# Performance work log

Measured on AMD Instinct MI355X. Metric: run time of the kernel, lower is better.

## Reference

```python
import jax, jax.numpy as jnp
import numpy as np

NEG_SLOPE = 0.2  # PyG GATConv default LeakyReLU negative slope
NUM_GRAPHS = 256


def gat_conv(x, edge_src, edge_dst, W, att_src, att_dst, bias):
    """PyG-style GATConv. x:[N,Fin], W:[H*C,Fin], att_*:[H,C], bias:[H*C]."""
    N = x.shape[0]
    H, C = att_src.shape
    h = (x @ W.T).reshape(N, H, C)                       # [N,H,C]
    a_src = jnp.sum(h * att_src, axis=-1)                # [N,H]
    a_dst = jnp.sum(h * att_dst, axis=-1)                # [N,H]
    e = jax.nn.leaky_relu(a_src[edge_src] + a_dst[edge_dst], NEG_SLOPE)  # [E,H]
    # segment softmax over edges sharing the same destination node
    m = jax.ops.segment_max(e, edge_dst, num_segments=N)
    ex = jnp.exp(e - m[edge_dst])
    den = jax.ops.segment_sum(ex, edge_dst, num_segments=N)
    alpha = ex / (den[edge_dst] + 1e-16)                 # [E,H]
    out = jax.ops.segment_sum(h[edge_src] * alpha[..., None], edge_dst,
                              num_segments=N)            # [N,H,C]
    return out.reshape(N, H * C) + bias


def setup_inputs() -> dict:
    key = jax.random.key(0)
    ks = jax.random.split(key, 16)
    N, E, Fin = 20000, 320000, 128
    H1, C1 = 8, 64          # conv1: heads=8, hidden_dim1=64 -> concat 512
    D1 = H1 * C1            # 512
    D2 = 128                # hidden_dim2, conv2 heads=1
    OUT = 2
    s = lambda k, shp, fan: jax.random.normal(k, shp, jnp.float32) * (1.0 / np.sqrt(fan))
    x = jax.random.normal(ks[0], (N, Fin), jnp.float32)
    edge_index = jax.random.randint(ks[1], (2, E), 0, N, jnp.int32)
    batch = jnp.sort(jax.random.randint(ks[2], (N,), 0, NUM_GRAPHS, jnp.int32))
    return {
        "x": x, "edge_index": edge_index, "batch": batch,
        "W1": s(ks[3], (D1, Fin), Fin), "att_src1": s(ks[4], (H1, C1), C1),
        "att_dst1": s(ks[5], (H1, C1), C1), "b1": jnp.zeros((D1,), jnp.float32),
        "W2": s(ks[6], (D2, D1), D1), "att_src2": s(ks[7], (1, D2), D2),
        "att_dst2": s(ks[8], (1, D2), D2), "b2": jnp.zeros((D2,), jnp.float32),
        "w_attn": s(ks[9], (D2, 1), D2), "b_attn": jnp.zeros((1,), jnp.float32),
        "w_mask": s(ks[10], (D2, 1), D2), "b_mask": jnp.zeros((1,), jnp.float32),
        "W_out": s(ks[11], (OUT, D2), D2), "b_out": jnp.zeros((OUT,), jnp.float32),
    }


def reference(x, edge_index, batch, W1, att_src1, att_dst1, b1,
              W2, att_src2, att_dst2, b2, w_attn, b_attn, w_mask, b_mask,
              W_out, b_out):
    N = x.shape[0]
    loops = jnp.arange(N, dtype=edge_index.dtype)
    src = jnp.concatenate([edge_index[0], loops])  # PyG add_self_loops=True
    dst = jnp.concatenate([edge_index[1], loops])

    h = gat_conv(x, src, dst, W1, att_src1, att_dst1, b1)   # [N, 512]
    h = jax.nn.relu(h)                                      # dropout = identity (eval)
    h = gat_conv(h, src, dst, W2, att_src2, att_dst2, b2)   # [N, 128]
    h = jax.nn.relu(h)

    # attention pooling over graphs in the batch
    attn_scores = h @ w_attn + b_attn                       # [N,1]
    node_mask = jax.nn.sigmoid(h @ w_mask + b_mask)         # [N,1]
    weighted = h * (attn_scores * node_mask)                # [N,128]
    pooled = jax.ops.segment_sum(weighted, batch, num_segments=NUM_GRAPHS)
    return pooled @ W_out.T + b_out                         # [256, 2]
```

## Files before the change

### kernel.cpp

```cpp
#include <hip/hip_runtime.h>
#include <math.h>


#define NEG_SLOPE 0.2f

using bf16x8 = __attribute__((ext_vector_type(8))) __bf16;
using f32x4  = __attribute__((ext_vector_type(4))) float;

__device__ __forceinline__ ushort f2bf(float f) {
    unsigned u = __float_as_uint(f);
    unsigned r = (u + 0x7FFFu + ((u >> 16) & 1u)) >> 16;
    return (ushort)r;
}
__device__ __forceinline__ unsigned pack2(float a, float b) {
    return (unsigned)f2bf(a) | ((unsigned)f2bf(b) << 16);
}
__device__ __forceinline__ void unpack8(uint4 u, float* f) {
    f[0] = __uint_as_float(u.x << 16); f[1] = __uint_as_float(u.x & 0xFFFF0000u);
    f[2] = __uint_as_float(u.y << 16); f[3] = __uint_as_float(u.y & 0xFFFF0000u);
    f[4] = __uint_as_float(u.z << 16); f[5] = __uint_as_float(u.z & 0xFFFF0000u);
    f[6] = __uint_as_float(u.w << 16); f[7] = __uint_as_float(u.w & 0xFFFF0000u);
}
__device__ __forceinline__ void unpack4(uint2 u, float* f) {
    f[0] = __uint_as_float(u.x << 16); f[1] = __uint_as_float(u.x & 0xFFFF0000u);
    f[2] = __uint_as_float(u.y << 16); f[3] = __uint_as_float(u.y & 0xFFFF0000u);
}

__global__ __launch_bounds__(256) void cvt_bf16(const float* __restrict__ in,
                                                ushort* __restrict__ out, int n4) {
    int i = blockIdx.x * 256 + threadIdx.x;
    if (i >= n4) return;
    float4 v = ((const float4*)in)[i];
    uint2 o;
    o.x = pack2(v.x, v.y);
    o.y = pack2(v.z, v.w);
    ((uint2*)out)[i] = o;
}

#define LDSB 40
__global__ __launch_bounds__(256) void gemm_mfma(const ushort* __restrict__ A,
                                                 const ushort* __restrict__ B,
                                                 ushort* __restrict__ C,
                                                 int M, int N, int K) {
    __shared__ ushort As[128 * LDSB];
    __shared__ ushort Bs[128 * LDSB];
    int t = threadIdx.x;
    int wave = t >> 6, lane = t & 63;
    int quad = lane >> 4, l16 = lane & 15;
    int m0 = blockIdx.x * 128;
    int n0 = blockIdx.y * 128;
    int wm = (wave & 1) * 64;
    int wn = (wave >> 1) * 64;
    int srow = t >> 1;
    int sseg = (t & 1) * 16;
    f32x4 acc[4][4] = {};
    for (int k0 = 0; k0 < K; k0 += 32) {
        uint4 av0, av1, bv0, bv1;
        {
            int grow = m0 + srow;
            if (grow < M) {
                const uint4* gp = (const uint4*)(A + (size_t)grow * K + k0 + sseg);
                av0 = gp[0]; av1 = gp[1];
            } else {
                av0 = make_uint4(0, 0, 0, 0); av1 = av0;
            }
            const uint4* gq = (const uint4*)(B + (size_t)(n0 + srow) * K + k0 + sseg);
            bv0 = gq[0]; bv1 = gq[1];
        }
        __syncthreads();
        *(uint4*)&As[srow * LDSB + sseg]     = av0;
        *(uint4*)&As[srow * LDSB + sseg + 8] = av1;
        *(uint4*)&Bs[srow * LDSB + sseg]     = bv0;
        *(uint4*)&Bs[srow * LDSB + sseg + 8] = bv1;
        __syncthreads();
        bf16x8 af[4], bf[4];
#pragma unroll
        for (int i = 0; i < 4; ++i)
            af[i] = *(const bf16x8*)&As[(wm + i * 16 + l16) * LDSB + quad * 8];
#pragma unroll
        for (int j = 0; j < 4; ++j)
            bf[j] = *(const bf16x8*)&Bs[(wn + j * 16 + l16) * LDSB + quad * 8];
#pragma unroll
        for (int i = 0; i < 4; ++i)
#pragma unroll
            for (int j = 0; j < 4; ++j)
                acc[i][j] = __builtin_amdgcn_mfma_f32_16x16x32_bf16(
                    af[i], bf[j], acc[i][j], 0, 0, 0);
    }
#pragma unroll
    for (int i = 0; i < 4; ++i) {
#pragma unroll
        for (int r = 0; r < 4; ++r) {
            int grow = m0 + wm + i * 16 + quad * 4 + r;
            if (grow < M) {
#pragma unroll
                for (int j = 0; j < 4; ++j) {
                    int gcol = n0 + wn + j * 16 + l16;
                    C[(size_t)grow * N + gcol] = f2bf(acc[i][j][r]);
                }
            }
        }
    }
}

__global__ __launch_bounds__(256) void scores1(const ushort* __restrict__ h1,
                                               const float* __restrict__ att_s,
                                               const float* __restrict__ att_d,
                                               float* __restrict__ a1s,
                                               float* __restrict__ a1d, int N) {
    int node = blockIdx.x * 4 + (threadIdx.x >> 6);
    if (node >= N) return;
    int lane = threadIdx.x & 63;
    uint4 u = *(const uint4*)(h1 + (size_t)node * 512 + lane * 8);
    float h[8];
    unpack8(u, h);
    const float4* sp = (const float4*)(att_s + lane * 8);
    const float4* dp = (const float4*)(att_d + lane * 8);
    float4 s0 = sp[0], s1 = sp[1], d0 = dp[0], d1 = dp[1];
    float ps = h[0] * s0.x + h[1] * s0.y + h[2] * s0.z + h[3] * s0.w +
               h[4] * s1.x + h[5] * s1.y + h[6] * s1.z + h[7] * s1.w;
    float pd = h[0] * d0.x + h[1] * d0.y + h[2] * d0.z + h[3] * d0.w +
               h[4] * d1.x + h[5] * d1.y + h[6] * d1.z + h[7] * d1.w;
#pragma unroll
    for (int off = 1; off < 8; off <<= 1) {
        ps += __shfl_xor(ps, off);
        pd += __shfl_xor(pd, off);
    }
    if ((lane & 7) == 0) {
        a1s[node * 8 + (lane >> 3)] = ps;
        a1d[node * 8 + (lane >> 3)] = pd;
    }
}

__global__ void count_edges(const int* __restrict__ dst, int* cnt, int E) {
    int e = blockIdx.x * 256 + threadIdx.x;
    if (e < E) atomicAdd(&cnt[dst[e]], 1);
}

__global__ __launch_bounds__(1024) void scan_offsets(const int* cnt, int* row_start,
                                                     int* cursor, int N) {
    __shared__ int sm[1024];
    int t = threadIdx.x;
    int per = (N + 1023) / 1024;
    int beg = t * per;
    int end = beg + per; if (end > N) end = N;
    int sum = 0;
    for (int i = beg; i < end; ++i) sum += cnt[i];
    sm[t] = sum;
    __syncthreads();
    for (int off = 1; off < 1024; off <<= 1) {
        int add = (t >= off) ? sm[t - off] : 0;
        __syncthreads();
        sm[t] += add;
        __syncthreads();
    }
    int run = sm[t] - sum;
    for (int i = beg; i < end; ++i) {
        int c = cnt[i];
        row_start[i] = run;
        cursor[i] = run;
        run += c;
    }
    if (t == 1023) row_start[N] = run;
}

__global__ void fill_edges(const int* __restrict__ src, const int* __restrict__ dst,
                           int* cursor, int* __restrict__ srcs, int E) {
    int e = blockIdx.x * 256 + threadIdx.x;
    if (e < E) {
        int pos = atomicAdd(&cursor[dst[e]], 1);
        srcs[pos] = src[e];
    }
}

__global__ __launch_bounds__(256) void agg1(const ushort* __restrict__ h1,
                                            const float* __restrict__ a1s,
                                            const float* __restrict__ a1d,
                                            const int* __restrict__ row_start,
                                            const int* __restrict__ srcs,
                                            const float* __restrict__ b1,
                                            ushort* __restrict__ r1, int N) {
    int node = blockIdx.x * 4 + (threadIdx.x >> 6);
    if (node >= N) return;
    int lane = threadIdx.x & 63;
    int head = lane >> 3;
    int f0 = lane * 8;
    int pbeg = row_start[node], pend = row_start[node + 1];
    float ad = a1d[node * 8 + head];
    float es = a1s[node * 8 + head] + ad;
    es = es > 0.f ? es : NEG_SLOPE * es;
    float ex_self = __expf(es);
    float den = ex_self;
    float q[8];
    unpack8(*(const uint4*)(h1 + (size_t)node * 512 + f0), q);
    float acc[8];
#pragma unroll
    for (int j = 0; j < 8; ++j) acc[j] = ex_self * q[j];
    int p = pbeg;
    for (; p + 4 <= pend; p += 4) {
        int s0 = srcs[p + 0];
        int s1 = srcs[p + 1];
        int s2 = srcs[p + 2];
        int s3 = srcs[p + 3];
        uint4 u0 = *(const uint4*)(h1 + (size_t)s0 * 512 + f0);
        uint4 u1 = *(const uint4*)(h1 + (size_t)s1 * 512 + f0);
        uint4 u2 = *(const uint4*)(h1 + (size_t)s2 * 512 + f0);
        uint4 u3 = *(const uint4*)(h1 + (size_t)s3 * 512 + f0);
        float as0 = a1s[s0 * 8 + head];
        float as1 = a1s[s1 * 8 + head];
        float as2 = a1s[s2 * 8 + head];
        float as3 = a1s[s3 * 8 + head];
        float e0 = as0 + ad; e0 = e0 > 0.f ? e0 : NEG_SLOPE * e0;
        float e1 = as1 + ad; e1 = e1 > 0.f ? e1 : NEG_SLOPE * e1;
        float e2 = as2 + ad; e2 = e2 > 0.f ? e2 : NEG_SLOPE * e2;
        float e3 = as3 + ad; e3 = e3 > 0.f ? e3 : NEG_SLOPE * e3;
        float x0 = __expf(e0), x1 = __expf(e1), x2 = __expf(e2), x3 = __expf(e3);
        den += (x0 + x1) + (x2 + x3);
        float v[8];
        unpack8(u0, v);
#pragma unroll
        for (int j = 0; j < 8; ++j) acc[j] += x0 * v[j];
        unpack8(u1, v);
#pragma unroll
        for (int j = 0; j < 8; ++j) acc[j] += x1 * v[j];
        unpack8(u2, v);
#pragma unroll
        for (int j = 0; j < 8; ++j) acc[j] += x2 * v[j];
        unpack8(u3, v);
#pragma unroll
        for (int j = 0; j < 8; ++j) acc[j] += x3 * v[j];
    }
    for (; p < pend; ++p) {
        int s = srcs[p];
        float e = a1s[s * 8 + head] + ad;
        e = e > 0.f ? e : NEG_SLOPE * e;
        float ex = __expf(e);
        den += ex;
        float v[8];
        unpack8(*(const uint4*)(h1 + (size_t)s * 512 + f0), v);
#pragma unroll
        for (int j = 0; j < 8; ++j) acc[j] += ex * v[j];
    }
    float rden = 1.0f / (den + 1e-16f);
    const float4* bp = (const float4*)(b1 + f0);
    float4 b0 = bp[0], b1v = bp[1];
    float o[8];
    o[0] = fmaxf(acc[0] * rden + b0.x, 0.f);
    o[1] = fmaxf(acc[1] * rden + b0.y, 0.f);
    o[2] = fmaxf(acc[2] * rden + b0.z, 0.f);
    o[3] = fmaxf(acc[3] * rden + b0.w, 0.f);
    o[4] = fmaxf(acc[4] * rden + b1v.x, 0.f);
    o[5] = fmaxf(acc[5] * rden + b1v.y, 0.f);
    o[6] = fmaxf(acc[6] * rden + b1v.z, 0.f);
    o[7] = fmaxf(acc[7] * rden + b1v.w, 0.f);
    uint4 ov;
    ov.x = pack2(o[0], o[1]); ov.y = pack2(o[2], o[3]);
    ov.z = pack2(o[4], o[5]); ov.w = pack2(o[6], o[7]);
    *(uint4*)(r1 + (size_t)node * 512 + f0) = ov;
}

__global__ __launch_bounds__(256) void scores2(const ushort* __restrict__ h2,
                                               const float* __restrict__ att_s,
                                               const float* __restrict__ att_d,
                                               float* __restrict__ a2s,
                                               float* __restrict__ a2d, int N) {
    int node = blockIdx.x * 4 + (threadIdx.x >> 6);
    if (node >= N) return;
    int lane = threadIdx.x & 63;
    unsigned u = *(const unsigned*)(h2 + (size_t)node * 128 + lane * 2);
    float h0 = __uint_as_float(u << 16), h1v = __uint_as_float(u & 0xFFFF0000u);
    float2 s = *(const float2*)(att_s + lane * 2);
    float2 d = *(const float2*)(att_d + lane * 2);
    float ps = h0 * s.x + h1v * s.y;
    float pd = h0 * d.x + h1v * d.y;
#pragma unroll
    for (int off = 1; off < 64; off <<= 1) {
        ps += __shfl_xor(ps, off);
        pd += __shfl_xor(pd, off);
    }
    if (lane == 0) { a2s[node] = ps; a2d[node] = pd; }
}

__global__ __launch_bounds__(256) void agg2(const ushort* __restrict__ h2,
                                            const float* __restrict__ a2s,
                                            const float* __restrict__ a2d,
                                            const int* __restrict__ row_start,
                                            const int* __restrict__ srcs,
                                            const float* __restrict__ b2,
                                            float* __restrict__ r2, int N) {
    int node = blockIdx.x * 8 + (threadIdx.x >> 5);
    if (node >= N) return;
    int sub = threadIdx.x & 31;
    int f0 = sub * 4;
    int pbeg = row_start[node], pend = row_start[node + 1];
    float ad = a2d[node];
    float es = a2s[node] + ad;
    es = es > 0.f ? es : NEG_SLOPE * es;
    float ex_self = __expf(es);
    float den = ex_self;
    float q[4];
    unpack4(*(const uint2*)(h2 + (size_t)node * 128 + f0), q);
    float acc[4];
#pragma unroll
    for (int j = 0; j < 4; ++j) acc[j] = ex_self * q[j];
    int p = pbeg;
    for (; p + 4 <= pend; p += 4) {
        int s0 = srcs[p + 0];
        int s1 = srcs[p + 1];
        int s2 = srcs[p + 2];
        int s3 = srcs[p + 3];
        uint2 u0 = *(const uint2*)(h2 + (size_t)s0 * 128 + f0);
        uint2 u1 = *(const uint2*)(h2 + (size_t)s1 * 128 + f0);
        uint2 u2 = *(const uint2*)(h2 + (size_t)s2 * 128 + f0);
        uint2 u3 = *(const uint2*)(h2 + (size_t)s3 * 128 + f0);
        float as0 = a2s[s0];
        float as1 = a2s[s1];
        float as2 = a2s[s2];
        float as3 = a2s[s3];
        float e0 = as0 + ad; e0 = e0 > 0.f ? e0 : NEG_SLOPE * e0;
        float e1 = as1 + ad; e1 = e1 > 0.f ? e1 : NEG_SLOPE * e1;
        float e2 = as2 + ad; e2 = e2 > 0.f ? e2 : NEG_SLOPE * e2;
        float e3 = as3 + ad; e3 = e3 > 0.f ? e3 : NEG_SLOPE * e3;
        float x0 = __expf(e0), x1 = __expf(e1), x2 = __expf(e2), x3 = __expf(e3);
        den += (x0 + x1) + (x2 + x3);
        float v[4];
        unpack4(u0, v);
#pragma unroll
        for (int j = 0; j < 4; ++j) acc[j] += x0 * v[j];
        unpack4(u1, v);
#pragma unroll
        for (int j = 0; j < 4; ++j) acc[j] += x1 * v[j];
        unpack4(u2, v);
#pragma unroll
        for (int j = 0; j < 4; ++j) acc[j] += x2 * v[j];
        unpack4(u3, v);
#pragma unroll
        for (int j = 0; j < 4; ++j) acc[j] += x3 * v[j];
    }
    for (; p < pend; ++p) {
        int s = srcs[p];
        float e = a2s[s] + ad;
        e = e > 0.f ? e : NEG_SLOPE * e;
        float ex = __expf(e);
        den += ex;
        float v[4];
        unpack4(*(const uint2*)(h2 + (size_t)s * 128 + f0), v);
#pragma unroll
        for (int j = 0; j < 4; ++j) acc[j] += ex * v[j];
    }
    float rden = 1.0f / (den + 1e-16f);
    float4 bv = *(const float4*)(b2 + f0);
    float4 o;
    o.x = fmaxf(acc[0] * rden + bv.x, 0.f);
    o.y = fmaxf(acc[1] * rden + bv.y, 0.f);
    o.z = fmaxf(acc[2] * rden + bv.z, 0.f);
    o.w = fmaxf(acc[3] * rden + bv.w, 0.f);
    *(float4*)(r2 + (size_t)node * 128 + f0) = o;
}

__global__ __launch_bounds__(256) void pool_kernel(const float* __restrict__ r2,
                                                   const int* __restrict__ batch,
                                                   const float* __restrict__ w_attn,
                                                   const float* __restrict__ b_attn,
                                                   const float* __restrict__ w_mask,
                                                   const float* __restrict__ b_mask,
                                                   float* pooled, int N) {
    int node = blockIdx.x * 4 + (threadIdx.x >> 6);
    if (node >= N) return;
    int lane = threadIdx.x & 63;
    float2 h = *(const float2*)(r2 + (size_t)node * 128 + lane * 2);
    float2 wa = *(const float2*)(w_attn + lane * 2);
    float2 wm = *(const float2*)(w_mask + lane * 2);
    float pa = h.x * wa.x + h.y * wa.y;
    float pm = h.x * wm.x + h.y * wm.y;
#pragma unroll
    for (int off = 1; off < 64; off <<= 1) {
        pa += __shfl_xor(pa, off);
        pm += __shfl_xor(pm, off);
    }
    float attn = pa + b_attn[0];
    float mask = 1.0f / (1.0f + __expf(-(pm + b_mask[0])));
    float w = attn * mask;
    int g = batch[node];
    atomicAdd(&pooled[g * 128 + lane * 2], h.x * w);
    atomicAdd(&pooled[g * 128 + lane * 2 + 1], h.y * w);
}

__global__ void final_kernel(const float* __restrict__ pooled,
                             const float* __restrict__ W_out,
                             const float* __restrict__ b_out,
                             float* __restrict__ out) {
    int tid = blockIdx.x * 256 + threadIdx.x;
    if (tid >= 512) return;
    int g = tid >> 1, o = tid & 1;
    const float* p = pooled + g * 128;
    const float* w = W_out + o * 128;
    float s = 0.f;
#pragma unroll 4
    for (int f = 0; f < 128; ++f) s += p[f] * w[f];
    out[tid] = s + b_out[o];
}

extern "C" void kernel_launch(void* const* d_in, const int* in_sizes, int n_in,
                              void* d_out, int out_size, void* d_ws, size_t ws_size,
                              hipStream_t stream) {
    const float* x        = (const float*)d_in[0];
    const int* edge_index = (const int*)d_in[1];
    const int* batch      = (const int*)d_in[2];
    const float* W1       = (const float*)d_in[3];
    const float* att_src1 = (const float*)d_in[4];
    const float* att_dst1 = (const float*)d_in[5];
    const float* b1       = (const float*)d_in[6];
    const float* W2       = (const float*)d_in[7];
    const float* att_src2 = (const float*)d_in[8];
    const float* att_dst2 = (const float*)d_in[9];
    const float* b2       = (const float*)d_in[10];
    const float* w_attn   = (const float*)d_in[11];
    const float* b_attn   = (const float*)d_in[12];
    const float* w_mask   = (const float*)d_in[13];
    const float* b_mask   = (const float*)d_in[14];
    const float* W_out    = (const float*)d_in[15];
    const float* b_out    = (const float*)d_in[16];
    float* out = (float*)d_out;

    int N = in_sizes[0] / 128;
    int E = in_sizes[1] / 2;
    const int* esrc = edge_index;
    const int* edst = edge_index + E;

    char* ws = (char*)d_ws;
    size_t off = 0;
    auto alloc = [&](size_t bytes) {
        void* p = ws + off;
        off = (off + bytes + 255) & ~(size_t)255;
        return p;
    };
    ushort* h1       = (ushort*)alloc((size_t)N * 512 * 2);
    ushort* r1       = (ushort*)alloc((size_t)N * 512 * 2);
    ushort* h2       = (ushort*)alloc((size_t)N * 128 * 2);
    float*  r2       = (float*)alloc((size_t)N * 128 * 4);
    ushort* xb       = (ushort*)alloc((size_t)N * 128 * 2);
    ushort* w1b      = (ushort*)alloc((size_t)512 * 128 * 2);
    ushort* w2b      = (ushort*)alloc((size_t)128 * 512 * 2);
    float*  a1s      = (float*)alloc((size_t)N * 8 * 4);
    float*  a1d      = (float*)alloc((size_t)N * 8 * 4);
    float*  a2s      = (float*)alloc((size_t)N * 4);
    float*  a2d      = (float*)alloc((size_t)N * 4);
    int*    row_start= (int*)alloc((size_t)(N + 1) * 4);
    int*    cursor   = (int*)alloc((size_t)N * 4);
    int*    srcs     = (int*)alloc((size_t)E * 4);
    float*  pooled   = (float*)alloc((size_t)256 * 128 * 4);

    hipMemsetAsync(cursor, 0, (size_t)N * 4, stream);
    hipMemsetAsync(pooled, 0, 256 * 128 * 4, stream);

    dim3 b256(256);
    int nx4 = N * 128 / 4;
    cvt_bf16<<<(nx4 + 255) / 256, b256, 0, stream>>>(x, xb, nx4);
    cvt_bf16<<<(512 * 128 / 4 + 255) / 256, b256, 0, stream>>>(W1, w1b, 512 * 128 / 4);
    cvt_bf16<<<(128 * 512 / 4 + 255) / 256, b256, 0, stream>>>(W2, w2b, 128 * 512 / 4);
    count_edges<<<(E + 255) / 256, b256, 0, stream>>>(edst, cursor, E);
    scan_offsets<<<1, 1024, 0, stream>>>(cursor, row_start, cursor, N);
    fill_edges<<<(E + 255) / 256, b256, 0, stream>>>(esrc, edst, cursor, srcs, E);
    gemm_mfma<<<dim3((N + 127) / 128, 512 / 128), b256, 0, stream>>>(xb, w1b, h1, N, 512, 128);
    scores1<<<(N + 3) / 4, b256, 0, stream>>>(h1, att_src1, att_dst1, a1s, a1d, N);
    agg1<<<(N + 3) / 4, b256, 0, stream>>>(h1, a1s, a1d, row_start, srcs, b1, r1, N);
    gemm_mfma<<<dim3((N + 127) / 128, 128 / 128), b256, 0, stream>>>(r1, w2b, h2, N, 128, 512);
    scores2<<<(N + 3) / 4, b256, 0, stream>>>(h2, att_src2, att_dst2, a2s, a2d, N);
    agg2<<<(N + 7) / 8, b256, 0, stream>>>(h2, a2s, a2d, row_start, srcs, b2, r2, N);
    pool_kernel<<<(N + 3) / 4, b256, 0, stream>>>(r2, batch, w_attn, b_attn, w_mask,
                                                  b_mask, pooled, N);
    final_kernel<<<2, b256, 0, stream>>>(pooled, W_out, b_out, out);
}
```

Before: 299.7 us.

## Fuse attention scores into GEMM epilogue, merge conversions, widen agg1 gather

Computes per-node attention source/destination scores inside the MFMA GEMM epilogue from fp32 accumulators, removing the separate scores1/scores2 kernels and their re-read of h. The three bf16 conversion launches are merged into one kernel, and the two memsets become one by reordering buffers contiguously. agg1's gather loop is restructured to issue eight predicated loads per iteration for more memory-level parallelism. Layer-2 scores now use atomics across four waves, and the scores are computed from unrounded accumulators, which changes numerics slightly.

```diff
diff --git a/kernel.cpp b/kernel.cpp
--- a/kernel.cpp
+++ b/kernel.cpp
@@ -15,33 +15,51 @@
 __device__ __forceinline__ unsigned pack2(float a, float b) {
     return (unsigned)f2bf(a) | ((unsigned)f2bf(b) << 16);
 }
+__device__ __forceinline__ float bflo(unsigned u) { return __uint_as_float(u << 16); }
+__device__ __forceinline__ float bfhi(unsigned u) { return __uint_as_float(u & 0xFFFF0000u); }
 __device__ __forceinline__ void unpack8(uint4 u, float* f) {
-    f[0] = __uint_as_float(u.x << 16); f[1] = __uint_as_float(u.x & 0xFFFF0000u);
-    f[2] = __uint_as_float(u.y << 16); f[3] = __uint_as_float(u.y & 0xFFFF0000u);
-    f[4] = __uint_as_float(u.z << 16); f[5] = __uint_as_float(u.z & 0xFFFF0000u);
-    f[6] = __uint_as_float(u.w << 16); f[7] = __uint_as_float(u.w & 0xFFFF0000u);
+    f[0] = bflo(u.x); f[1] = bfhi(u.x);
+    f[2] = bflo(u.y); f[3] = bfhi(u.y);
+    f[4] = bflo(u.z); f[5] = bfhi(u.z);
+    f[6] = bflo(u.w); f[7] = bfhi(u.w);
 }
 __device__ __forceinline__ void unpack4(uint2 u, float* f) {
-    f[0] = __uint_as_float(u.x << 16); f[1] = __uint_as_float(u.x & 0xFFFF0000u);
-    f[2] = __uint_as_float(u.y << 16); f[3] = __uint_as_float(u.y & 0xFFFF0000u);
-}
-
-__global__ __launch_bounds__(256) void cvt_bf16(const float* __restrict__ in,
-                                                ushort* __restrict__ out, int n4) {
+    f[0] = bflo(u.x); f[1] = bfhi(u.x);
+    f[2] = bflo(u.y); f[3] = bfhi(u.y);
+}
+
+__global__ __launch_bounds__(256) void cvt3(const float* __restrict__ x, ushort* __restrict__ xb, int nx4,
+                                            const float* __restrict__ w1, ushort* __restrict__ w1b, int nw14,
+                                            const float* __restrict__ w2, ushort* __restrict__ w2b, int nw24) {
     int i = blockIdx.x * 256 + threadIdx.x;
-    if (i >= n4) return;
-    float4 v = ((const float4*)in)[i];
+    const float* src; ushort* dst; int j = i;
+    if (j < nx4) { src = x; dst = xb; }
+    else {
+        j -= nx4;
+        if (j < nw14) { src = w1; dst = w1b; }
+        else {
+            j -= nw14;
+            if (j >= nw24) return;
+            src = w2; dst = w2b;
+        }
+    }
+    float4 v = ((const float4*)src)[j];
     uint2 o;
     o.x = pack2(v.x, v.y);
     o.y = pack2(v.z, v.w);
-    ((uint2*)out)[i] = o;
+    ((uint2*)dst)[j] = o;
 }
 
 #define LDSB 40
 __global__ __launch_bounds__(256) void gemm_mfma(const ushort* __restrict__ A,
                                                  const ushort* __restrict__ B,
                                                  ushort* __restrict__ C,
-                                                 int M, int N, int K) {
+                                                 int M, int N, int K,
+                                                 const float* __restrict__ att_s,
+                                                 const float* __restrict__ att_d,
+                                                 float* __restrict__ sout,
+                                                 float* __restrict__ dout,
+                                                 int H) {
     __shared__ ushort As[128 * LDSB];
     __shared__ ushort Bs[128 * LDSB];
     int t = threadIdx.x;
@@ -101,34 +119,38 @@
             }
         }
     }
-}
-
-__global__ __launch_bounds__(256) void scores1(const ushort* __restrict__ h1,
-                                               const float* __restrict__ att_s,
-                                               const float* __restrict__ att_d,
-                                               float* __restrict__ a1s,
-                                               float* __restrict__ a1d, int N) {
-    int node = blockIdx.x * 4 + (threadIdx.x >> 6);
-    if (node >= N) return;
-    int lane = threadIdx.x & 63;
-    uint4 u = *(const uint4*)(h1 + (size_t)node * 512 + lane * 8);
-    float h[8];
-    unpack8(u, h);
-    const float4* sp = (const float4*)(att_s + lane * 8);
-    const float4* dp = (const float4*)(att_d + lane * 8);
-    float4 s0 = sp[0], s1 = sp[1], d0 = dp[0], d1 = dp[1];
-    float ps = h[0] * s0.x + h[1] * s0.y + h[2] * s0.z + h[3] * s0.w +
-               h[4] * s1.x + h[5] * s1.y + h[6] * s1.z + h[7] * s1.w;
-    float pd = h[0] * d0.x + h[1] * d0.y + h[2] * d0.z + h[3] * d0.w +
-               h[4] * d1.x + h[5] * d1.y + h[6] * d1.z + h[7] * d1.w;
-#pragma unroll
-    for (int off = 1; off < 8; off <<= 1) {
-        ps += __shfl_xor(ps, off);
-        pd += __shfl_xor(pd, off);
-    }
-    if ((lane & 7) == 0) {
-        a1s[node * 8 + (lane >> 3)] = ps;
-        a1d[node * 8 + (lane >> 3)] = pd;
+    float as[4], adw[4];
+#pragma unroll
+    for (int j = 0; j < 4; ++j) {
+        int col = n0 + wn + j * 16 + l16;
+        as[j]  = att_s[col];
+        adw[j] = att_d[col];
+    }
+    int head = (H == 8) ? ((n0 + wn) >> 6) : 0;
+#pragma unroll
+    for (int i = 0; i < 4; ++i) {
+#pragma unroll
+        for (int r = 0; r < 4; ++r) {
+            float ps = acc[i][0][r] * as[0] + acc[i][1][r] * as[1] +
+                       acc[i][2][r] * as[2] + acc[i][3][r] * as[3];
+            float pd = acc[i][0][r] * adw[0] + acc[i][1][r] * adw[1] +
+                       acc[i][2][r] * adw[2] + acc[i][3][r] * adw[3];
+#pragma unroll
+            for (int off = 1; off < 16; off <<= 1) {
+                ps += __shfl_xor(ps, off);
+                pd += __shfl_xor(pd, off);
+            }
+            int grow = m0 + wm + i * 16 + quad * 4 + r;
+            if (l16 == 0 && grow < M) {
+                if (H == 1) {
+                    atomicAdd(&sout[grow], ps);
+                    atomicAdd(&dout[grow], pd);
+                } else {
+                    sout[grow * 8 + head] = ps;
+                    dout[grow * 8 + head] = pd;
+                }
+            }
+        }
     }
 }
 
@@ -196,50 +218,32 @@
     float acc[8];
 #pragma unroll
     for (int j = 0; j < 8; ++j) acc[j] = ex_self * q[j];
-    int p = pbeg;
-    for (; p + 4 <= pend; p += 4) {
-        int s0 = srcs[p + 0];
-        int s1 = srcs[p + 1];
-        int s2 = srcs[p + 2];
-        int s3 = srcs[p + 3];
-        uint4 u0 = *(const uint4*)(h1 + (size_t)s0 * 512 + f0);
-        uint4 u1 = *(const uint4*)(h1 + (size_t)s1 * 512 + f0);
-        uint4 u2 = *(const uint4*)(h1 + (size_t)s2 * 512 + f0);
-        uint4 u3 = *(const uint4*)(h1 + (size_t)s3 * 512 + f0);
-        float as0 = a1s[s0 * 8 + head];
-        float as1 = a1s[s1 * 8 + head];
-        float as2 = a1s[s2 * 8 + head];
-        float as3 = a1s[s3 * 8 + head];
-        float e0 = as0 + ad; e0 = e0 > 0.f ? e0 : NEG_SLOPE * e0;
-        float e1 = as1 + ad; e1 = e1 > 0.f ? e1 : NEG_SLOPE * e1;
-        float e2 = as2 + ad; e2 = e2 > 0.f ? e2 : NEG_SLOPE * e2;
-        float e3 = as3 + ad; e3 = e3 > 0.f ? e3 : NEG_SLOPE * e3;
-        float x0 = __expf(e0), x1 = __expf(e1), x2 = __expf(e2), x3 = __expf(e3);
-        den += (x0 + x1) + (x2 + x3);
-        float v[8];
-        unpack8(u0, v);
-#pragma unroll
-        for (int j = 0; j < 8; ++j) acc[j] += x0 * v[j];
-        unpack8(u1, v);
-#pragma unroll
-        for (int j = 0; j < 8; ++j) acc[j] += x1 * v[j];
-        unpack8(u2, v);
-#pragma unroll
-        for (int j = 0; j < 8; ++j) acc[j] += x2 * v[j];
-        unpack8(u3, v);
-#pragma unroll
-        for (int j = 0; j < 8; ++j) acc[j] += x3 * v[j];
-    }
-    for (; p < pend; ++p) {
-        int s = srcs[p];
-        float e = a1s[s * 8 + head] + ad;
-        e = e > 0.f ? e : NEG_SLOPE * e;
-        float ex = __expf(e);
-        den += ex;
-        float v[8];
-        unpack8(*(const uint4*)(h1 + (size_t)s * 512 + f0), v);
-#pragma unroll
-        for (int j = 0; j < 8; ++j) acc[j] += ex * v[j];
+    for (int p = pbeg; p < pend; p += 8) {
+        int sidx[8]; bool okb[8];
+#pragma unroll
+        for (int k = 0; k < 8; ++k) {
+            int pk = p + k;
+            okb[k] = pk < pend;
+            sidx[k] = srcs[okb[k] ? pk : pbeg];
+        }
+        uint4 u[8];
+#pragma unroll
+        for (int k = 0; k < 8; ++k)
+            u[k] = *(const uint4*)(h1 + (size_t)sidx[k] * 512 + f0);
+        float sc[8];
+#pragma unroll
+        for (int k = 0; k < 8; ++k) sc[k] = a1s[sidx[k] * 8 + head];
+#pragma unroll
+        for (int k = 0; k < 8; ++k) {
+            float e = sc[k] + ad;
+            e = e > 0.f ? e : NEG_SLOPE * e;
+            float xk = okb[k] ? __expf(e) : 0.f;
+            den += xk;
+            float v[8];
+            unpack8(u[k], v);
+#pragma unroll
+            for (int j = 0; j < 8; ++j) acc[j] += xk * v[j];
+        }
     }
     float rden = 1.0f / (den + 1e-16f);
     const float4* bp = (const float4*)(b1 + f0);
@@ -257,28 +261,6 @@
     ov.x = pack2(o[0], o[1]); ov.y = pack2(o[2], o[3]);
     ov.z = pack2(o[4], o[5]); ov.w = pack2(o[6], o[7]);
     *(uint4*)(r1 + (size_t)node * 512 + f0) = ov;
-}
-
-__global__ __launch_bounds__(256) void scores2(const ushort* __restrict__ h2,
-                                               const float* __restrict__ att_s,
-                                               const float* __restrict__ att_d,
-                                               float* __restrict__ a2s,
-                                               float* __restrict__ a2d, int N) {
-    int node = blockIdx.x * 4 + (threadIdx.x >> 6);
-    if (node >= N) return;
-    int lane = threadIdx.x & 63;
-    unsigned u = *(const unsigned*)(h2 + (size_t)node * 128 + lane * 2);
-    float h0 = __uint_as_float(u << 16), h1v = __uint_as_float(u & 0xFFFF0000u);
-    float2 s = *(const float2*)(att_s + lane * 2);
-    float2 d = *(const float2*)(att_d + lane * 2);
-    float ps = h0 * s.x + h1v * s.y;
-    float pd = h0 * d.x + h1v * d.y;
-#pragma unroll
-    for (int off = 1; off < 64; off <<= 1) {
-        ps += __shfl_xor(ps, off);
-        pd += __shfl_xor(pd, off);
-    }
-    if (lane == 0) { a2s[node] = ps; a2d[node] = pd; }
 }
 
 __global__ __launch_bounds__(256) void agg2(const ushort* __restrict__ h2,
@@ -444,29 +426,28 @@
     ushort* w2b      = (ushort*)alloc((size_t)128 * 512 * 2);
     float*  a1s      = (float*)alloc((size_t)N * 8 * 4);
     float*  a1d      = (float*)alloc((size_t)N * 8 * 4);
+    int*    row_start= (int*)alloc((size_t)(N + 1) * 4);
+    int*    srcs     = (int*)alloc((size_t)E * 4);
+    int*    cursor   = (int*)alloc((size_t)N * 4);
     float*  a2s      = (float*)alloc((size_t)N * 4);
     float*  a2d      = (float*)alloc((size_t)N * 4);
-    int*    row_start= (int*)alloc((size_t)(N + 1) * 4);
-    int*    cursor   = (int*)alloc((size_t)N * 4);
-    int*    srcs     = (int*)alloc((size_t)E * 4);
     float*  pooled   = (float*)alloc((size_t)256 * 128 * 4);
-
-    hipMemsetAsync(cursor, 0, (size_t)N * 4, stream);
-    hipMemsetAsync(pooled, 0, 256 * 128 * 4, stream);
+    size_t zspan = (size_t)((char*)(pooled + 256 * 128) - (char*)cursor);
+    hipMemsetAsync(cursor, 0, zspan, stream);
 
     dim3 b256(256);
     int nx4 = N * 128 / 4;
-    cvt_bf16<<<(nx4 + 255) / 256, b256, 0, stream>>>(x, xb, nx4);
-    cvt_bf16<<<(512 * 128 / 4 + 255) / 256, b256, 0, stream>>>(W1, w1b, 512 * 128 / 4);
-    cvt_bf16<<<(128 * 512 / 4 + 255) / 256, b256, 0, stream>>>(W2, w2b, 128 * 512 / 4);
+    int nw4 = 512 * 128 / 4;
+    cvt3<<<(nx4 + 2 * nw4 + 255) / 256, b256, 0, stream>>>(x, xb, nx4, W1, w1b, nw4,
+                                                           W2, w2b, nw4);
     count_edges<<<(E + 255) / 256, b256, 0, stream>>>(edst, cursor, E);
     scan_offsets<<<1, 1024, 0, stream>>>(cursor, row_start, cursor, N);
     fill_edges<<<(E + 255) / 256, b256, 0, stream>>>(esrc, edst, cursor, srcs, E);
-    gemm_mfma<<<dim3((N + 127) / 128, 512 / 128), b256, 0, stream>>>(xb, w1b, h1, N, 512, 128);
-    scores1<<<(N + 3) / 4, b256, 0, stream>>>(h1, att_src1, att_dst1, a1s, a1d, N);
+    gemm_mfma<<<dim3((N + 127) / 128, 512 / 128), b256, 0, stream>>>(
+        xb, w1b, h1, N, 512, 128, att_src1, att_dst1, a1s, a1d, 8);
     agg1<<<(N + 3) / 4, b256, 0, stream>>>(h1, a1s, a1d, row_start, srcs, b1, r1, N);
-    gemm_mfma<<<dim3((N + 127) / 128, 128 / 128), b256, 0, stream>>>(r1, w2b, h2, N, 128, 512);
-    scores2<<<(N + 3) / 4, b256, 0, stream>>>(h2, att_src2, att_dst2, a2s, a2d, N);
+    gemm_mfma<<<dim3((N + 127) / 128, 128 / 128), b256, 0, stream>>>(
+        r1, w2b, h2, N, 128, 512, att_src2, att_dst2, a2s, a2d, 1);
     agg2<<<(N + 7) / 8, b256, 0, stream>>>(h2, a2s, a2d, row_start, srcs, b2, r2, N);
     pool_kernel<<<(N + 3) / 4, b256, 0, stream>>>(r2, batch, w_attn, b_attn, w_mask,
                                                   b_mask, pooled, N);
```

Measured after the change: 294.1 us. Within noise of the previous version (-1.9%).
